# Kernel tuning notes

Hardware: AMD Instinct MI355X
Metric: run time of the kernel (lower is better)

Reference implementation:

```python
import jax, jax.numpy as jnp
import numpy as np

N_NODES = 50000
IN_CH = 128
OUT_CH = 64
N_EDGES = 800000
K_HOPS = 2


def setup_inputs() -> dict:
    key = jax.random.key(0)
    k1, k2, k3, k4 = jax.random.split(key, 4)
    x = jax.random.normal(k1, (N_NODES, IN_CH), dtype=jnp.float32)
    edge_index = jax.random.randint(k2, (2, N_EDGES), 0, N_NODES, dtype=jnp.int64)
    # SGC linear layer params (torch Linear default init approx)
    scale = 1.0 / np.sqrt(IN_CH)
    W = jax.random.uniform(k3, (IN_CH, OUT_CH), dtype=jnp.float32, minval=-scale, maxval=scale)
    b = jax.random.uniform(k4, (OUT_CH,), dtype=jnp.float32, minval=-scale, maxval=scale)
    return {"x": x, "edge_index": edge_index, "W": W, "b": b}


def _sgc_propagate(x, row, col, K):
    # GCN symmetric normalization with self-loops: S = D^-1/2 (A+I) D^-1/2
    n = x.shape[0]
    loop = jnp.arange(n, dtype=row.dtype)
    row = jnp.concatenate([row, loop])
    col = jnp.concatenate([col, loop])
    ones = jnp.ones(row.shape[0], dtype=x.dtype)
    deg = jax.ops.segment_sum(ones, col, num_segments=n)
    dinv = jnp.where(deg > 0, jax.lax.rsqrt(deg), 0.0)
    norm = dinv[row] * dinv[col]  # [E+N]
    for _ in range(K):
        # gather source features, weight, scatter-add to targets
        msg = norm[:, None] * x[row]  # [E+N, C]
        x = jax.ops.segment_sum(msg, col, num_segments=n)
    return x


def reference(x, edge_index, W, b):
    # Dropout is identity in eval mode (deterministic reference).
    row, col = edge_index[0], edge_index[1]
    h = _sgc_propagate(x, row, col, K_HOPS)  # [N, IN_CH]
    return h @ W + b  # [N, OUT_CH]
```

## Files before the change

kernel.cpp:

```cpp
#include <hip/hip_runtime.h>

#define N_NODES 50000
#define IN_CH   128
#define OUT_CH  64
#define N_EDGES 800000
#define NBINS   49
#define LBCAP   128
#define BINCAP  20000
#define PCAP    64
#define WT_STR  136
#define SA_B    500
#define SA_E    1600
#define SB_B    49
#define GEMM_BL 196
#define HOP_NB  782
#define ZPL     (N_NODES * 4)
#define YT_STR  68


using short8  = __attribute__((ext_vector_type(8))) short;
using float4v = __attribute__((ext_vector_type(4))) float;
using uint4v  = __attribute__((ext_vector_type(4))) unsigned int;

__device__ __forceinline__ unsigned int bpack(float a, float b) {
    unsigned int ua = __float_as_uint(a), ub = __float_as_uint(b);
    unsigned int ra = (ua + 0x7fffu + ((ua >> 16) & 1u)) >> 16;
    unsigned int rb = (ub + 0x7fffu + ((ub >> 16) & 1u)) & 0xffff0000u;
    return (ra & 0xffffu) | rb;
}

__global__ __launch_bounds__(256) void scatter_a(const int* __restrict__ row,
        const int* __restrict__ col, unsigned int* __restrict__ binbuf,
        int* __restrict__ gcur, int* __restrict__ deg32) {
    __shared__ unsigned int sbuf[NBINS][LBCAP];
    __shared__ int scnt[NBINS];
    __shared__ int sdst[NBINS];
    const int tid = threadIdx.x;
    if (tid < NBINS) scnt[tid] = 0;
    __syncthreads();
    const int e0 = blockIdx.x * SA_E;
    for (int i = tid; i < SA_E / 4; i += 256) {
        int e = e0 + i * 4;
        int4 t4 = *(const int4*)&col[e];
        int4 s4 = *(const int4*)&row[e];
        const int ts[4] = { t4.x, t4.y, t4.z, t4.w };
        const int ss[4] = { s4.x, s4.y, s4.z, s4.w };
        #pragma unroll
        for (int j = 0; j < 4; ++j) {
            int b = ts[j] >> 10;
            atomicAdd(&deg32[ts[j]], 1);
            int pos = atomicAdd(&scnt[b], 1);
            if (pos < LBCAP)
                sbuf[b][pos] = ((unsigned)(ts[j] & 1023) << 16) | (unsigned)ss[j];
        }
    }
    __syncthreads();
    if (tid < NBINS) {
        int c = scnt[tid]; if (c > LBCAP) c = LBCAP; scnt[tid] = c;
        sdst[tid] = atomicAdd(&gcur[tid], c);
    }
    __syncthreads();
    const int wave = tid >> 6, lane = tid & 63;
    for (int b = wave; b < NBINS; b += 4) {
        int c = scnt[b];
        size_t d = (size_t)b * BINCAP + sdst[b];
        for (int i = lane; i < c; i += 64)
            binbuf[d + i] = sbuf[b][i];
    }
}

__global__ __launch_bounds__(1024) void scatb_gemm(
        const unsigned int* __restrict__ binbuf, const int* __restrict__ gcur,
        unsigned short* __restrict__ esrc, const int* __restrict__ deg32,
        const float* __restrict__ x, const float* __restrict__ W,
        uint4v* __restrict__ z0) {
    const int bid = blockIdx.x, tid = threadIdx.x;
    if (bid < SB_B) {
        __shared__ int lcnt[1024];
        const int t0 = bid << 10;
        lcnt[tid] = 0;
        __syncthreads();
        int cnt = gcur[bid]; if (cnt > BINCAP) cnt = BINCAP;
        const unsigned int* src = binbuf + (size_t)bid * BINCAP;
        for (int i = tid; i < cnt; i += 1024) {
            unsigned int e = src[i];
            int tl = e >> 16;
            int pos = atomicAdd(&lcnt[tl], 1);
            int t = t0 + tl;
            if (pos < PCAP && t < N_NODES)
                esrc[(size_t)pos * N_NODES + t] = (unsigned short)(e & 0xffffu);
        }
        return;
    }
    __shared__ unsigned short sWT[64 * WT_STR];
    __shared__ float ytile[16 * 16 * YT_STR];
    for (int i = tid; i < IN_CH * OUT_CH; i += 1024) {
        int k = i >> 6, c = i & 63;
        unsigned int u = __float_as_uint(W[i]);
        u = (u + 0x7fffu + ((u >> 16) & 1u)) >> 16;
        sWT[c * WT_STR + k] = (unsigned short)u;
    }
    __syncthreads();
    const int lane = tid & 63;
    const int quad = lane >> 4;
    const int c15  = lane & 15;
    const int wid  = tid >> 6;
    const int tile = (bid - SB_B) * 16 + wid;
    if (tile >= N_NODES / 16) return;

    short8 bf[4][4];
    #pragma unroll
    for (int t = 0; t < 4; ++t)
        #pragma unroll
        for (int ch = 0; ch < 4; ++ch)
            bf[ch][t] = *(const short8*)&sWT[(t * 16 + c15) * WT_STR + ch * 32 + quad * 8];

    const float* xr = x + ((size_t)tile * 16 + c15) * IN_CH;
    float4v acc[4] = {{0.f,0.f,0.f,0.f},{0.f,0.f,0.f,0.f},
                      {0.f,0.f,0.f,0.f},{0.f,0.f,0.f,0.f}};
    #pragma unroll
    for (int ch = 0; ch < 4; ++ch) {
        float4 f0 = *(const float4*)(xr + ch * 32 + quad * 8);
        float4 f1 = *(const float4*)(xr + ch * 32 + quad * 8 + 4);
        unsigned int d0 = bpack(f0.x, f0.y), d1 = bpack(f0.z, f0.w);
        unsigned int d2 = bpack(f1.x, f1.y), d3 = bpack(f1.z, f1.w);
        short8 a8;
        a8[0] = (short)d0; a8[1] = (short)(d0 >> 16);
        a8[2] = (short)d1; a8[3] = (short)(d1 >> 16);
        a8[4] = (short)d2; a8[5] = (short)(d2 >> 16);
        a8[6] = (short)d3; a8[7] = (short)(d3 >> 16);
        #pragma unroll
        for (int t = 0; t < 4; ++t)
            acc[t] = __builtin_amdgcn_mfma_f32_16x16x32_bf16(a8, bf[ch][t], acc[t], 0, 0, 0);
    }
    float* yt = &ytile[wid * (16 * YT_STR)];
    #pragma unroll
    for (int t = 0; t < 4; ++t)
        #pragma unroll
        for (int r = 0; r < 4; ++r)
            yt[(quad * 4 + r) * YT_STR + t * 16 + c15] = acc[t][r];
    #pragma unroll
    for (int k = 0; k < 2; ++k) {
        int u = lane + 64 * k;
        int node = u >> 3, j = u & 7;
        int half = j >> 2, qq = j & 3;
        const float* src = &yt[node * YT_STR + j * 8];
        float4 f0 = *(const float4*)src;
        float4 f1 = *(const float4*)(src + 4);
        int n = tile * 16 + node;
        float dv = rsqrtf((float)(deg32[n] + 1));
        uint4v pk;
        pk.x = bpack(dv * f0.x, dv * f0.y);
        pk.y = bpack(dv * f0.z, dv * f0.w);
        pk.z = bpack(dv * f1.x, dv * f1.y);
        pk.w = bpack(dv * f1.z, dv * f1.w);
        __builtin_nontemporal_store(pk, z0 + (size_t)half * ZPL + (size_t)n * 4 + qq);
    }
}

__global__ __launch_bounds__(256) void hop_gather(const uint4v* __restrict__ hin,
        void* __restrict__ hout, const int* __restrict__ deg32,
        const unsigned short* __restrict__ esrc, const float* __restrict__ bias,
        int last) {
    const int half = blockIdx.x & 1;
    const int wg   = blockIdx.x >> 1;
    const int lane = threadIdx.x & 63;
    const int r    = lane >> 2;
    const int q    = lane & 3;
    const int t    = wg * 64 + (threadIdx.x >> 6) * 16 + r;
    if (t >= N_NODES) return;
    int deg = deg32[t]; if (deg > PCAP) deg = PCAP;
    const uint4v* hp = hin + (size_t)half * ZPL;

    uint4v rr = hp[t * 4 + q];
    float acc[8];
    {
        const unsigned int rw[4] = { rr.x, rr.y, rr.z, rr.w };
        #pragma unroll
        for (int j = 0; j < 4; ++j) {
            acc[2 * j]     = __uint_as_float(rw[j] << 16);
            acc[2 * j + 1] = __uint_as_float(rw[j] & 0xffff0000u);
        }
    }
    int e = 0;
    int s = (0 < deg) ? (int)esrc[t] : -1;
    while (__any(s >= 0)) {
        int sn = (e + 1 < deg) ? (int)esrc[(size_t)(e + 1) * N_NODES + t] : -1;
        if (s >= 0) {
            uint4v v = hp[s * 4 + q];
            const unsigned int rw[4] = { v.x, v.y, v.z, v.w };
            #pragma unroll
            for (int j = 0; j < 4; ++j) {
                acc[2 * j]     += __uint_as_float(rw[j] << 16);
                acc[2 * j + 1] += __uint_as_float(rw[j] & 0xffff0000u);
            }
        }
        s = sn; ++e;
    }

    if (!last) {
        float rdeg = 1.0f / (float)(deg + 1);
        uint4v pk;
        pk.x = bpack(acc[0] * rdeg, acc[1] * rdeg);
        pk.y = bpack(acc[2] * rdeg, acc[3] * rdeg);
        pk.z = bpack(acc[4] * rdeg, acc[5] * rdeg);
        pk.w = bpack(acc[6] * rdeg, acc[7] * rdeg);
        __builtin_nontemporal_store(pk,
            (uint4v*)hout + (size_t)half * ZPL + t * 4 + q);
    } else {
        float d = rsqrtf((float)(deg + 1));
        float4 b0 = ((const float4*)bias)[half * 8 + q * 2];
        float4 b1 = ((const float4*)bias)[half * 8 + q * 2 + 1];
        float4v o0 = { d * acc[0] + b0.x, d * acc[1] + b0.y,
                       d * acc[2] + b0.z, d * acc[3] + b0.w };
        float4v o1 = { d * acc[4] + b1.x, d * acc[5] + b1.y,
                       d * acc[6] + b1.z, d * acc[7] + b1.w };
        __builtin_nontemporal_store(o0, (float4v*)hout + t * 16 + half * 8 + q * 2);
        __builtin_nontemporal_store(o1, (float4v*)hout + t * 16 + half * 8 + q * 2 + 1);
    }
}

extern "C" void kernel_launch(void* const* d_in, const int* in_sizes, int n_in,
                              void* d_out, int out_size, void* d_ws, size_t ws_size,
                              hipStream_t stream) {
    const float* x  = (const float*)d_in[0];
    const int*   ei = (const int*)d_in[1];
    const float* W  = (const float*)d_in[2];
    const float* b  = (const float*)d_in[3];
    float*       out = (float*)d_out;

    const int* row = ei;
    const int* col = ei + N_EDGES;

    char* ws = (char*)d_ws;
    size_t a = 0;
    auto alloc = [&](size_t bytes) { char* p = ws + a; a = (a + bytes + 255) & ~(size_t)255; return p; };
    int*            gcur   = (int*)           alloc(NBINS * sizeof(int));
    int*            deg32  = (int*)           alloc((size_t)N_NODES * sizeof(int));
    unsigned int*   binbuf = (unsigned int*)  alloc((size_t)NBINS * BINCAP * 4);
    unsigned short* esrc   = (unsigned short*)alloc((size_t)PCAP * N_NODES * 2);
    unsigned int*   z0     = (unsigned int*)  alloc((size_t)N_NODES * OUT_CH * 2);
    unsigned int*   z1     = (unsigned int*)  alloc((size_t)N_NODES * OUT_CH * 2);

    hipMemsetAsync(gcur, 0, 256 + (size_t)N_NODES * sizeof(int), stream);

    const int B = 256;
    int gH = 2 * HOP_NB;

    scatter_a<<<SA_B, B, 0, stream>>>(row, col, binbuf, gcur, deg32);
    scatb_gemm<<<SB_B + GEMM_BL, 1024, 0, stream>>>(binbuf, gcur, esrc, deg32, x, W,
                                                    (uint4v*)z0);
    hop_gather<<<gH, B, 0, stream>>>((const uint4v*)z0, (void*)z1, deg32, esrc, b, 0);
    hop_gather<<<gH, B, 0, stream>>>((const uint4v*)z1, (void*)out, deg32, esrc, b, 1);
}
```

Measured before the change: 172.1 us.

## Fuse edge binning, bucket scatter and GEMM into one kernel with flags

Merges the edge-binning kernel and the scatter/GEMM kernel into a single launch whose block groups synchronise through global atomic flags with spin-waits. Degrees are now counted per bin in shared memory instead of with global atomics per edge, which also removes the large deg32 memset. The GEMM blocks do their MFMA work before waiting on the flag, so the transform overlaps with the binning. In exchange it depends on all 370 blocks being co-resident (spin-waits could deadlock otherwise), uses larger per-block shared buffers, and adds a second pass over each bin.

```diff
diff --git a/kernel.cpp b/kernel.cpp
--- a/kernel.cpp
+++ b/kernel.cpp
@@ -5,17 +5,20 @@
 #define OUT_CH  64
 #define N_EDGES 800000
 #define NBINS   49
-#define LBCAP   128
 #define BINCAP  20000
 #define PCAP    64
 #define WT_STR  136
-#define SA_B    500
-#define SA_E    1600
-#define SB_B    49
-#define GEMM_BL 196
+#define MEGA_A  125
+#define A_EDGES 6400
+#define LBCAP2  256
+#define MEGA_B  49
+#define MEGA_G  196
+#define MEGA_NB (MEGA_A + MEGA_B + MEGA_G)
 #define HOP_NB  782
 #define ZPL     (N_NODES * 4)
 #define YT_STR  68
+#define FLAG_A  56
+#define FLAG_B  57
 
 
 using short8  = __attribute__((ext_vector_type(8))) short;
@@ -29,71 +32,95 @@
     return (ra & 0xffffu) | rb;
 }
 
-__global__ __launch_bounds__(256) void scatter_a(const int* __restrict__ row,
+__global__ __launch_bounds__(1024) void mega(const int* __restrict__ row,
         const int* __restrict__ col, unsigned int* __restrict__ binbuf,
-        int* __restrict__ gcur, int* __restrict__ deg32) {
-    __shared__ unsigned int sbuf[NBINS][LBCAP];
-    __shared__ int scnt[NBINS];
-    __shared__ int sdst[NBINS];
-    const int tid = threadIdx.x;
-    if (tid < NBINS) scnt[tid] = 0;
-    __syncthreads();
-    const int e0 = blockIdx.x * SA_E;
-    for (int i = tid; i < SA_E / 4; i += 256) {
-        int e = e0 + i * 4;
-        int4 t4 = *(const int4*)&col[e];
-        int4 s4 = *(const int4*)&row[e];
-        const int ts[4] = { t4.x, t4.y, t4.z, t4.w };
-        const int ss[4] = { s4.x, s4.y, s4.z, s4.w };
-        #pragma unroll
-        for (int j = 0; j < 4; ++j) {
-            int b = ts[j] >> 10;
-            atomicAdd(&deg32[ts[j]], 1);
-            int pos = atomicAdd(&scnt[b], 1);
-            if (pos < LBCAP)
-                sbuf[b][pos] = ((unsigned)(ts[j] & 1023) << 16) | (unsigned)ss[j];
-        }
-    }
-    __syncthreads();
-    if (tid < NBINS) {
-        int c = scnt[tid]; if (c > LBCAP) c = LBCAP; scnt[tid] = c;
-        sdst[tid] = atomicAdd(&gcur[tid], c);
-    }
-    __syncthreads();
-    const int wave = tid >> 6, lane = tid & 63;
-    for (int b = wave; b < NBINS; b += 4) {
-        int c = scnt[b];
-        size_t d = (size_t)b * BINCAP + sdst[b];
-        for (int i = lane; i < c; i += 64)
-            binbuf[d + i] = sbuf[b][i];
-    }
-}
-
-__global__ __launch_bounds__(1024) void scatb_gemm(
-        const unsigned int* __restrict__ binbuf, const int* __restrict__ gcur,
-        unsigned short* __restrict__ esrc, const int* __restrict__ deg32,
-        const float* __restrict__ x, const float* __restrict__ W,
-        uint4v* __restrict__ z0) {
+        int* __restrict__ gcur, unsigned short* __restrict__ esrc,
+        int* __restrict__ deg32, const float* __restrict__ x,
+        const float* __restrict__ W, uint4v* __restrict__ z0) {
+    __shared__ alignas(16) char smem[69632];
     const int bid = blockIdx.x, tid = threadIdx.x;
-    if (bid < SB_B) {
-        __shared__ int lcnt[1024];
-        const int t0 = bid << 10;
+
+    if (bid < MEGA_A) {
+        unsigned int* sbuf = (unsigned int*)smem;
+        int* scnt = (int*)(smem + NBINS * LBCAP2 * 4);
+        int* sdst = scnt + 64;
+        if (tid < NBINS) scnt[tid] = 0;
+        __syncthreads();
+        const int e0 = bid * A_EDGES;
+        for (int i = tid; i < A_EDGES / 4; i += 1024) {
+            int e = e0 + i * 4;
+            int4 t4 = *(const int4*)&col[e];
+            int4 s4 = *(const int4*)&row[e];
+            const int ts[4] = { t4.x, t4.y, t4.z, t4.w };
+            const int ss[4] = { s4.x, s4.y, s4.z, s4.w };
+            #pragma unroll
+            for (int j = 0; j < 4; ++j) {
+                int b = ts[j] >> 10;
+                int pos = atomicAdd(&scnt[b], 1);
+                if (pos < LBCAP2)
+                    sbuf[b * LBCAP2 + pos] =
+                        ((unsigned)(ts[j] & 1023) << 16) | (unsigned)ss[j];
+            }
+        }
+        __syncthreads();
+        if (tid < NBINS) {
+            int c = scnt[tid]; if (c > LBCAP2) c = LBCAP2; scnt[tid] = c;
+            sdst[tid] = atomicAdd(&gcur[tid], c);
+        }
+        __syncthreads();
+        const int wave = tid >> 6, lane = tid & 63;
+        for (int b = wave; b < NBINS; b += 16) {
+            int c = scnt[b];
+            size_t d = (size_t)b * BINCAP + sdst[b];
+            for (int i = lane; i < c; i += 64)
+                binbuf[d + i] = sbuf[b * LBCAP2 + i];
+        }
+        __syncthreads();
+        __threadfence();
+        if (tid == 0)
+            __hip_atomic_fetch_add(&gcur[FLAG_A], 1, __ATOMIC_RELEASE,
+                                   __HIP_MEMORY_SCOPE_AGENT);
+        return;
+    }
+
+    if (bid < MEGA_A + MEGA_B) {
+        int* lcnt = (int*)smem;
+        const int bin = bid - MEGA_A;
+        const int t0 = bin << 10;
+        if (tid == 0) {
+            while (__hip_atomic_load(&gcur[FLAG_A], __ATOMIC_ACQUIRE,
+                                     __HIP_MEMORY_SCOPE_AGENT) < MEGA_A)
+                __builtin_amdgcn_s_sleep(8);
+        }
         lcnt[tid] = 0;
         __syncthreads();
-        int cnt = gcur[bid]; if (cnt > BINCAP) cnt = BINCAP;
-        const unsigned int* src = binbuf + (size_t)bid * BINCAP;
+        int cnt = gcur[bin]; if (cnt > BINCAP) cnt = BINCAP;
+        const unsigned int* src = binbuf + (size_t)bin * BINCAP;
+        for (int i = tid; i < cnt; i += 1024)
+            atomicAdd(&lcnt[src[i] >> 16], 1);
+        __syncthreads();
+        int t = t0 + tid;
+        if (t < N_NODES) deg32[t] = lcnt[tid];
+        __syncthreads();
+        __threadfence();
+        if (tid == 0)
+            __hip_atomic_fetch_add(&gcur[FLAG_B], 1, __ATOMIC_RELEASE,
+                                   __HIP_MEMORY_SCOPE_AGENT);
+        lcnt[tid] = 0;
+        __syncthreads();
         for (int i = tid; i < cnt; i += 1024) {
             unsigned int e = src[i];
             int tl = e >> 16;
             int pos = atomicAdd(&lcnt[tl], 1);
-            int t = t0 + tl;
-            if (pos < PCAP && t < N_NODES)
-                esrc[(size_t)pos * N_NODES + t] = (unsigned short)(e & 0xffffu);
+            int tt = t0 + tl;
+            if (pos < PCAP && tt < N_NODES)
+                esrc[(size_t)pos * N_NODES + tt] = (unsigned short)(e & 0xffffu);
         }
         return;
     }
-    __shared__ unsigned short sWT[64 * WT_STR];
-    __shared__ float ytile[16 * 16 * YT_STR];
+
+    unsigned short* sWT = (unsigned short*)smem;
+    float* ytile = (float*)smem;
     for (int i = tid; i < IN_CH * OUT_CH; i += 1024) {
         int k = i >> 6, c = i & 63;
         unsigned int u = __float_as_uint(W[i]);
@@ -105,34 +132,43 @@
     const int quad = lane >> 4;
     const int c15  = lane & 15;
     const int wid  = tid >> 6;
-    const int tile = (bid - SB_B) * 16 + wid;
-    if (tile >= N_NODES / 16) return;
+    const int tile = (bid - MEGA_A - MEGA_B) * 16 + wid;
+    const bool active = tile < (N_NODES / 16);
 
     short8 bf[4][4];
-    #pragma unroll
-    for (int t = 0; t < 4; ++t)
-        #pragma unroll
-        for (int ch = 0; ch < 4; ++ch)
-            bf[ch][t] = *(const short8*)&sWT[(t * 16 + c15) * WT_STR + ch * 32 + quad * 8];
-
-    const float* xr = x + ((size_t)tile * 16 + c15) * IN_CH;
     float4v acc[4] = {{0.f,0.f,0.f,0.f},{0.f,0.f,0.f,0.f},
                       {0.f,0.f,0.f,0.f},{0.f,0.f,0.f,0.f}};
-    #pragma unroll
-    for (int ch = 0; ch < 4; ++ch) {
-        float4 f0 = *(const float4*)(xr + ch * 32 + quad * 8);
-        float4 f1 = *(const float4*)(xr + ch * 32 + quad * 8 + 4);
-        unsigned int d0 = bpack(f0.x, f0.y), d1 = bpack(f0.z, f0.w);
-        unsigned int d2 = bpack(f1.x, f1.y), d3 = bpack(f1.z, f1.w);
-        short8 a8;
-        a8[0] = (short)d0; a8[1] = (short)(d0 >> 16);
-        a8[2] = (short)d1; a8[3] = (short)(d1 >> 16);
-        a8[4] = (short)d2; a8[5] = (short)(d2 >> 16);
-        a8[6] = (short)d3; a8[7] = (short)(d3 >> 16);
+    if (active) {
         #pragma unroll
         for (int t = 0; t < 4; ++t)
-            acc[t] = __builtin_amdgcn_mfma_f32_16x16x32_bf16(a8, bf[ch][t], acc[t], 0, 0, 0);
-    }
+            #pragma unroll
+            for (int ch = 0; ch < 4; ++ch)
+                bf[ch][t] = *(const short8*)&sWT[(t * 16 + c15) * WT_STR + ch * 32 + quad * 8];
+
+        const float* xr = x + ((size_t)tile * 16 + c15) * IN_CH;
+        #pragma unroll
+        for (int ch = 0; ch < 4; ++ch) {
+            float4 f0 = *(const float4*)(xr + ch * 32 + quad * 8);
+            float4 f1 = *(const float4*)(xr + ch * 32 + quad * 8 + 4);
+            unsigned int d0 = bpack(f0.x, f0.y), d1 = bpack(f0.z, f0.w);
+            unsigned int d2 = bpack(f1.x, f1.y), d3 = bpack(f1.z, f1.w);
+            short8 a8;
+            a8[0] = (short)d0; a8[1] = (short)(d0 >> 16);
+            a8[2] = (short)d1; a8[3] = (short)(d1 >> 16);
+            a8[4] = (short)d2; a8[5] = (short)(d2 >> 16);
+            a8[6] = (short)d3; a8[7] = (short)(d3 >> 16);
+            #pragma unroll
+            for (int t = 0; t < 4; ++t)
+                acc[t] = __builtin_amdgcn_mfma_f32_16x16x32_bf16(a8, bf[ch][t], acc[t], 0, 0, 0);
+        }
+    }
+    if (tid == 0) {
+        while (__hip_atomic_load(&gcur[FLAG_B], __ATOMIC_ACQUIRE,
+                                 __HIP_MEMORY_SCOPE_AGENT) < MEGA_B)
+            __builtin_amdgcn_s_sleep(8);
+    }
+    __syncthreads();
+    if (!active) return;
     float* yt = &ytile[wid * (16 * YT_STR)];
     #pragma unroll
     for (int t = 0; t < 4; ++t)
@@ -144,9 +180,9 @@
         int u = lane + 64 * k;
         int node = u >> 3, j = u & 7;
         int half = j >> 2, qq = j & 3;
-        const float* src = &yt[node * YT_STR + j * 8];
-        float4 f0 = *(const float4*)src;
-        float4 f1 = *(const float4*)(src + 4);
+        const float* srcp = &yt[node * YT_STR + j * 8];
+        float4 f0 = *(const float4*)srcp;
+        float4 f1 = *(const float4*)(srcp + 4);
         int n = tile * 16 + node;
         float dv = rsqrtf((float)(deg32[n] + 1));
         uint4v pk;
@@ -235,21 +271,20 @@
     char* ws = (char*)d_ws;
     size_t a = 0;
     auto alloc = [&](size_t bytes) { char* p = ws + a; a = (a + bytes + 255) & ~(size_t)255; return p; };
-    int*            gcur   = (int*)           alloc(NBINS * sizeof(int));
+    int*            gcur   = (int*)           alloc(64 * sizeof(int));
     int*            deg32  = (int*)           alloc((size_t)N_NODES * sizeof(int));
     unsigned int*   binbuf = (unsigned int*)  alloc((size_t)NBINS * BINCAP * 4);
     unsigned short* esrc   = (unsigned short*)alloc((size_t)PCAP * N_NODES * 2);
     unsigned int*   z0     = (unsigned int*)  alloc((size_t)N_NODES * OUT_CH * 2);
     unsigned int*   z1     = (unsigned int*)  alloc((size_t)N_NODES * OUT_CH * 2);
 
-    hipMemsetAsync(gcur, 0, 256 + (size_t)N_NODES * sizeof(int), stream);
+    hipMemsetAsync(gcur, 0, 256, stream);
 
     const int B = 256;
     int gH = 2 * HOP_NB;
 
-    scatter_a<<<SA_B, B, 0, stream>>>(row, col, binbuf, gcur, deg32);
-    scatb_gemm<<<SB_B + GEMM_BL, 1024, 0, stream>>>(binbuf, gcur, esrc, deg32, x, W,
-                                                    (uint4v*)z0);
+    mega<<<MEGA_NB, 1024, 0, stream>>>(row, col, binbuf, gcur, esrc, deg32, x, W,
+                                       (uint4v*)z0);
     hop_gather<<<gH, B, 0, stream>>>((const uint4v*)z0, (void*)z1, deg32, esrc, b, 0);
     hop_gather<<<gH, B, 0, stream>>>((const uint4v*)z1, (void*)out, deg32, esrc, b, 1);
 }
```

Result: slower. 250.6 us (+45.6%).
